# Kernel tuning notes

Hardware: AMD Instinct MI355X
Metric: run time of the kernel (lower is better)

Reference implementation:

```python
import jax, jax.numpy as jnp
import numpy as np

B, C, H, W = 2, 64, 512, 512
HEADS = 4
EPS = 1e-12  # F.normalize eps


def setup_inputs() -> dict:
    key = jax.random.key(0)
    ks = jax.random.split(key, 7)
    s = 0.02
    return {
        "x": jax.random.normal(ks[0], (B, C, H, W), jnp.float32),
        "Wq": jax.random.normal(ks[1], (C, C), jnp.float32) * s,
        "Wk": jax.random.normal(ks[2], (C, C), jnp.float32) * s,
        "Wv": jax.random.normal(ks[3], (C, C), jnp.float32) * s,
        "Wp": jax.random.normal(ks[4], (C, C), jnp.float32) * s,
        "bp": jax.random.normal(ks[5], (C,), jnp.float32) * s,
        "rescale": jnp.ones((HEADS, 1, 1), jnp.float32),
    }


def reference(x, Wq, Wk, Wv, Wp, bp, rescale):
    b, c, h, w = x.shape
    n = h * w
    d = c // HEADS
    xf = x.reshape(b, c, n)  # 1x1 conv == channel matmul on flattened spatial

    def conv1x1(Wt):
        return jnp.einsum('oc,bcn->bon', Wt, xf)

    # torch: permute->reshape(b,n,c)->split heads->transpose == reshape conv out to (b,heads,d,n)
    q = conv1x1(Wq).reshape(b, HEADS, d, n)
    k = conv1x1(Wk).reshape(b, HEADS, d, n)
    v = conv1x1(Wv).reshape(b, HEADS, d, n)

    def l2norm(t):  # F.normalize(p=2, dim=-1)
        nrm = jnp.sqrt(jnp.sum(t * t, axis=-1, keepdims=True))
        return t / jnp.maximum(nrm, EPS)

    q = l2norm(q)
    k = l2norm(k)

    attn = jnp.einsum('bhdn,bhen->bhde', k, q)  # (b, heads, d, d) tiny matrix
    attn = attn * rescale  # rescale broadcasts (heads,1,1)
    attn = jax.nn.softmax(attn, axis=-1)

    o = jnp.einsum('bhde,bhen->bhdn', attn, v).reshape(b, c, n)
    out = jnp.einsum('oc,bcn->bon', Wp, o) + bp[None, :, None] + xf  # proj + residual
    return out.reshape(b, c, h, w)
```

## Files before the change

kernel.cpp:

```cpp
#include <hip/hip_runtime.h>
#include <math.h>

#define C 64
#define NHEADS 4
#define DH 16
#define NN 262144
#define NB 2
#define PB 512
#define NT 2
#define EPS 1e-12f

typedef __attribute__((ext_vector_type(8))) short short8v;
typedef __attribute__((ext_vector_type(8))) unsigned short ushort8v;
typedef __attribute__((ext_vector_type(4))) unsigned short ushort4v;
typedef __attribute__((ext_vector_type(4))) float f32x4;

static __device__ __forceinline__ unsigned short f2bf(float f) {
  union { float f; unsigned int u; } v; v.f = f;
  unsigned int r = v.u + 0x7fffu + ((v.u >> 16) & 1u);
  return (unsigned short)(r >> 16);
}

__global__ __launch_bounds__(256, 2) void gram_kernel(const float* __restrict__ x,
                                                      float* __restrict__ Gc) {
  __shared__ unsigned short xs[C * 256];
  const int b = blockIdx.y;
  const int chunk = blockIdx.x;
  const float* xb = x + (size_t)b * C * NN;
  const int t = threadIdx.x;
  const int w = t >> 6, l = t & 63;
  const int lrow = l & 15, lhi = l >> 4;

  const int gA0 = (w >> 1) * 2, gA1 = gA0 + 1;
  const int gB0 = (w & 1) * 2,  gB1 = gB0 + 1;
  const int cA0 = gA0 * 16 + lrow, cA1 = gA1 * 16 + lrow;
  const int cB0 = gB0 * 16 + lrow, cB1 = gB1 * 16 + lrow;

  f32x4 acc0 = {0.f,0.f,0.f,0.f}, acc1 = {0.f,0.f,0.f,0.f};
  f32x4 acc2 = {0.f,0.f,0.f,0.f}, acc3 = {0.f,0.f,0.f,0.f};

  for (int tile = 0; tile < NT; ++tile) {
    const int j0 = (chunk * NT + tile) * 256;
    __syncthreads();
#pragma unroll
    for (int i = 0; i < 8; ++i) {
      const int oi = i * 256 + t;
      const int c = oi >> 5, oct = oi & 31;
      const float* src = xb + (size_t)c * NN + j0 + oct * 8;
      const float4 v0 = *reinterpret_cast<const float4*>(src);
      const float4 v1 = *reinterpret_cast<const float4*>(src + 4);
      ushort8v pk;
      pk[0] = f2bf(v0.x); pk[1] = f2bf(v0.y); pk[2] = f2bf(v0.z); pk[3] = f2bf(v0.w);
      pk[4] = f2bf(v1.x); pk[5] = f2bf(v1.y); pk[6] = f2bf(v1.z); pk[7] = f2bf(v1.w);
      *reinterpret_cast<ushort8v*>(&xs[c * 256 + ((oct ^ (c & 7)) << 3)]) = pk;
    }
    __syncthreads();
#pragma unroll
    for (int s = 0; s < 8; ++s) {
      const int o = s * 4 + lhi;
      const short8v fA0 = *reinterpret_cast<const short8v*>(&xs[cA0 * 256 + ((o ^ (cA0 & 7)) << 3)]);
      const short8v fA1 = *reinterpret_cast<const short8v*>(&xs[cA1 * 256 + ((o ^ (cA1 & 7)) << 3)]);
      const short8v fB0 = *reinterpret_cast<const short8v*>(&xs[cB0 * 256 + ((o ^ (cB0 & 7)) << 3)]);
      const short8v fB1 = *reinterpret_cast<const short8v*>(&xs[cB1 * 256 + ((o ^ (cB1 & 7)) << 3)]);
      acc0 = __builtin_amdgcn_mfma_f32_16x16x32_bf16(fA0, fB0, acc0, 0, 0, 0);
      acc1 = __builtin_amdgcn_mfma_f32_16x16x32_bf16(fA0, fB1, acc1, 0, 0, 0);
      acc2 = __builtin_amdgcn_mfma_f32_16x16x32_bf16(fA1, fB0, acc2, 0, 0, 0);
      acc3 = __builtin_amdgcn_mfma_f32_16x16x32_bf16(fA1, fB1, acc3, 0, 0, 0);
    }
  }
  float* g = Gc + ((size_t)b * PB + chunk) * 4096;
#pragma unroll
  for (int r = 0; r < 4; ++r) {
    const int row = lhi * 4 + r;
    g[(gA0 * 16 + row) * 64 + gB0 * 16 + lrow] = acc0[r];
    g[(gA0 * 16 + row) * 64 + gB1 * 16 + lrow] = acc1[r];
    g[(gA1 * 16 + row) * 64 + gB0 * 16 + lrow] = acc2[r];
    g[(gA1 * 16 + row) * 64 + gB1 * 16 + lrow] = acc3[r];
  }
}

__global__ __launch_bounds__(256) void reduce_kernel(const float* __restrict__ Gc,
                                                     float* __restrict__ G) {
  __shared__ float s[4][64];
  const int b = blockIdx.y;
  const int g = blockIdx.x;
  const int t = threadIdx.x;
  const int e = g * 64 + (t & 63);
  const int chunk = t >> 6;
  float sum = 0.f;
  for (int p = chunk; p < PB; p += 4)
    sum += Gc[((size_t)b * PB + p) * 4096 + e];
  s[chunk][t & 63] = sum;
  __syncthreads();
  if (t < 64) G[(size_t)b * 4096 + g * 64 + t] = s[0][t] + s[1][t] + s[2][t] + s[3][t];
}

__global__ __launch_bounds__(256) void attn_kernel(const float* __restrict__ G,
    const float* __restrict__ Wq, const float* __restrict__ Wk,
    const float* __restrict__ Wv, const float* __restrict__ Wp,
    const float* __restrict__ rescale, unsigned short* __restrict__ Ebf) {
  __shared__ float Gs[4096], GQt[4096], GKt[4096], T[4096];
  __shared__ float attnw[64][DH];
  __shared__ float nq[64], nk[64];
  const int b = blockIdx.x;
  const int t = threadIdx.x;

  for (int i = t; i < 4096; i += 256) Gs[i] = G[(size_t)b * 4096 + i];
  __syncthreads();
  for (int i = t; i < 4096; i += 256) {
    const int c = i >> 6, e = i & 63;
    float sq_ = 0.f, sk_ = 0.f;
    for (int c2 = 0; c2 < 64; ++c2) {
      const float g = Gs[c * 64 + c2];
      sq_ += g * Wq[e * 64 + c2];
      sk_ += g * Wk[e * 64 + c2];
    }
    GQt[c * 64 + e] = sq_;
    GKt[c * 64 + e] = sk_;
  }
  __syncthreads();
  if (t < 64) {
    float s = 0.f;
    for (int c2 = 0; c2 < 64; ++c2) s += Wq[t * 64 + c2] * GQt[c2 * 64 + t];
    nq[t] = sqrtf(fmaxf(s, 0.f));
  } else if (t < 128) {
    const int d = t - 64;
    float s = 0.f;
    for (int c2 = 0; c2 < 64; ++c2) s += Wk[d * 64 + c2] * GKt[c2 * 64 + d];
    nk[d] = sqrtf(fmaxf(s, 0.f));
  }
  __syncthreads();
  if (t < 64) {
    const int h = t >> 4;
    const float rs = rescale[h];
    const float nkd = fmaxf(nk[t], EPS);
    float logits[DH];
    float mx = -1e30f;
    for (int ee = 0; ee < DH; ++ee) {
      const int e = h * DH + ee;
      float num = 0.f;
      for (int c2 = 0; c2 < 64; ++c2) num += Wk[t * 64 + c2] * GQt[c2 * 64 + e];
      const float l = num / (nkd * fmaxf(nq[e], EPS)) * rs;
      logits[ee] = l;
      mx = fmaxf(mx, l);
    }
    float sum = 0.f;
    for (int ee = 0; ee < DH; ++ee) { const float p = expf(logits[ee] - mx); logits[ee] = p; sum += p; }
    const float inv = 1.f / sum;
    for (int ee = 0; ee < DH; ++ee) attnw[t][ee] = logits[ee] * inv;
  }
  __syncthreads();
  for (int i = t; i < 4096; i += 256) {
    const int r = i >> 6, c = i & 63;
    const int h = r >> 4;
    float s = 0.f;
    for (int e = 0; e < DH; ++e) s += attnw[r][e] * Wv[(h * DH + e) * 64 + c];
    T[i] = s;
  }
  __syncthreads();
  for (int i = t; i < 4096; i += 256) {
    const int r = i >> 6, c = i & 63;
    float s = (r == c) ? 1.f : 0.f;
    for (int m = 0; m < 64; ++m) s += Wp[r * 64 + m] * T[m * 64 + c];
    Ebf[(size_t)b * 4096 + i] = f2bf(s);
  }
}

__global__ __launch_bounds__(256, 4) void apply_kernel(const float* __restrict__ x,
    const unsigned short* __restrict__ Ebf, const float* __restrict__ bp,
    float* __restrict__ out) {
  __shared__ unsigned short xt[128 * 64];
  const int b = blockIdx.y;
  const int n0 = blockIdx.x * 128;
  const float* xb = x + (size_t)b * C * NN;
  float* ob = out + (size_t)b * C * NN;
  const int t = threadIdx.x;
  const int w = t >> 6, l = t & 63;
  const int lrow = l & 15, lhi = l >> 4;

  short8v ef[4][2];
  const unsigned short* eb = Ebf + (size_t)b * 4096;
#pragma unroll
  for (int ot = 0; ot < 4; ++ot)
#pragma unroll
    for (int ks = 0; ks < 2; ++ks)
      ef[ot][ks] = *reinterpret_cast<const short8v*>(eb + (ot * 16 + lrow) * 64 + ks * 32 + lhi * 8);

#pragma unroll
  for (int h = 0; h < 2; ++h) {
    const int n = h * 64 + l;
#pragma unroll
    for (int i = 0; i < 4; ++i) {
      const int c0 = w * 16 + i * 4;
      const float v0 = xb[(size_t)(c0 + 0) * NN + n0 + n];
      const float v1 = xb[(size_t)(c0 + 1) * NN + n0 + n];
      const float v2 = xb[(size_t)(c0 + 2) * NN + n0 + n];
      const float v3 = xb[(size_t)(c0 + 3) * NN + n0 + n];
      ushort4v pk;
      pk[0] = f2bf(v0); pk[1] = f2bf(v1); pk[2] = f2bf(v2); pk[3] = f2bf(v3);
      const int q = c0 >> 2;
      *reinterpret_cast<ushort4v*>(
          &xt[n * 64 + ((((q >> 1) ^ (n & 7)) << 3) + (q & 1) * 4)]) = pk;
    }
  }
  __syncthreads();

  f32x4 acc[4][2];
#pragma unroll
  for (int ot = 0; ot < 4; ++ot)
#pragma unroll
    for (int nn = 0; nn < 2; ++nn) acc[ot][nn] = (f32x4){0.f, 0.f, 0.f, 0.f};

  const int nbase = w * 32;
#pragma unroll
  for (int nn = 0; nn < 2; ++nn) {
    const int n = nbase + nn * 16 + lrow;
#pragma unroll
    for (int ks = 0; ks < 2; ++ks) {
      const int s = ks * 4 + lhi;
      const short8v xf = *reinterpret_cast<const short8v*>(&xt[n * 64 + ((s ^ (n & 7)) << 3)]);
#pragma unroll
      for (int ot = 0; ot < 4; ++ot)
        acc[ot][nn] = __builtin_amdgcn_mfma_f32_16x16x32_bf16(ef[ot][ks], xf, acc[ot][nn], 0, 0, 0);
    }
  }

#pragma unroll
  for (int ot = 0; ot < 4; ++ot) {
#pragma unroll
    for (int r = 0; r < 4; ++r) {
      const int o = ot * 16 + lhi * 4 + r;
      const float bias = bp[o];
#pragma unroll
      for (int nn = 0; nn < 2; ++nn) {
        const int n = nbase + nn * 16 + lrow;
        ob[(size_t)o * NN + n0 + n] = acc[ot][nn][r] + bias;
      }
    }
  }
}

extern "C" void kernel_launch(void* const* d_in, const int* in_sizes, int n_in,
                              void* d_out, int out_size, void* d_ws, size_t ws_size,
                              hipStream_t stream) {
  const float* x       = (const float*)d_in[0];
  const float* Wq      = (const float*)d_in[1];
  const float* Wk      = (const float*)d_in[2];
  const float* Wv      = (const float*)d_in[3];
  const float* Wp      = (const float*)d_in[4];
  const float* bp      = (const float*)d_in[5];
  const float* rescale = (const float*)d_in[6];
  float* out = (float*)d_out;

  float* Gc = out;
  float* G  = (float*)d_ws;
  unsigned short* Ebf = (unsigned short*)(G + (size_t)NB * 4096);

  gram_kernel<<<dim3(PB, NB), dim3(256), 0, stream>>>(x, Gc);
  reduce_kernel<<<dim3(64, NB), dim3(256), 0, stream>>>(Gc, G);
  attn_kernel<<<dim3(NB), dim3(256), 0, stream>>>(G, Wq, Wk, Wv, Wp, rescale, Ebf);
  apply_kernel<<<dim3(2048, NB), dim3(256), 0, stream>>>(x, Ebf, bp, out);
}
```

Baseline: 155.7 us.

## Rewrite apply kernel as persistent per-wave streaming without LDS staging

Replaces the LDS-staged apply kernel with a grid-stride persistent kernel in which each wave handles 32-pixel chunks. Inputs are loaded straight into MFMA operand registers, and the operand order is swapped so that the accumulator layout allows float4 vectorized output stores. This removes the shared-memory transpose and the block barrier, and cuts the grid to 384x2 blocks. In exchange, the per-lane global loads are 4-byte strided across channels, each covering only 16 contiguous pixels, which may hurt coalescing. Occupancy is lower because the launch bound drops from 4 to 3 blocks.

```diff
diff --git a/kernel.cpp b/kernel.cpp
--- a/kernel.cpp
+++ b/kernel.cpp
@@ -12,7 +12,6 @@
 
 typedef __attribute__((ext_vector_type(8))) short short8v;
 typedef __attribute__((ext_vector_type(8))) unsigned short ushort8v;
-typedef __attribute__((ext_vector_type(4))) unsigned short ushort4v;
 typedef __attribute__((ext_vector_type(4))) float f32x4;
 
 static __device__ __forceinline__ unsigned short f2bf(float f) {
@@ -166,12 +165,10 @@
   }
 }
 
-__global__ __launch_bounds__(256, 4) void apply_kernel(const float* __restrict__ x,
+__global__ __launch_bounds__(256, 3) void apply_stream(const float* __restrict__ x,
     const unsigned short* __restrict__ Ebf, const float* __restrict__ bp,
     float* __restrict__ out) {
-  __shared__ unsigned short xt[128 * 64];
   const int b = blockIdx.y;
-  const int n0 = blockIdx.x * 128;
   const float* xb = x + (size_t)b * C * NN;
   float* ob = out + (size_t)b * C * NN;
   const int t = threadIdx.x;
@@ -186,55 +183,51 @@
     for (int ks = 0; ks < 2; ++ks)
       ef[ot][ks] = *reinterpret_cast<const short8v*>(eb + (ot * 16 + lrow) * 64 + ks * 32 + lhi * 8);
 
-#pragma unroll
-  for (int h = 0; h < 2; ++h) {
-    const int n = h * 64 + l;
-#pragma unroll
-    for (int i = 0; i < 4; ++i) {
-      const int c0 = w * 16 + i * 4;
-      const float v0 = xb[(size_t)(c0 + 0) * NN + n0 + n];
-      const float v1 = xb[(size_t)(c0 + 1) * NN + n0 + n];
-      const float v2 = xb[(size_t)(c0 + 2) * NN + n0 + n];
-      const float v3 = xb[(size_t)(c0 + 3) * NN + n0 + n];
-      ushort4v pk;
-      pk[0] = f2bf(v0); pk[1] = f2bf(v1); pk[2] = f2bf(v2); pk[3] = f2bf(v3);
-      const int q = c0 >> 2;
-      *reinterpret_cast<ushort4v*>(
-          &xt[n * 64 + ((((q >> 1) ^ (n & 7)) << 3) + (q & 1) * 4)]) = pk;
-    }
-  }
-  __syncthreads();
-
-  f32x4 acc[4][2];
-#pragma unroll
-  for (int ot = 0; ot < 4; ++ot)
-#pragma unroll
-    for (int nn = 0; nn < 2; ++nn) acc[ot][nn] = (f32x4){0.f, 0.f, 0.f, 0.f};
-
-  const int nbase = w * 32;
-#pragma unroll
-  for (int nn = 0; nn < 2; ++nn) {
-    const int n = nbase + nn * 16 + lrow;
-#pragma unroll
-    for (int ks = 0; ks < 2; ++ks) {
-      const int s = ks * 4 + lhi;
-      const short8v xf = *reinterpret_cast<const short8v*>(&xt[n * 64 + ((s ^ (n & 7)) << 3)]);
-#pragma unroll
-      for (int ot = 0; ot < 4; ++ot)
-        acc[ot][nn] = __builtin_amdgcn_mfma_f32_16x16x32_bf16(ef[ot][ks], xf, acc[ot][nn], 0, 0, 0);
-    }
-  }
-
-#pragma unroll
-  for (int ot = 0; ot < 4; ++ot) {
-#pragma unroll
-    for (int r = 0; r < 4; ++r) {
-      const int o = ot * 16 + lhi * 4 + r;
-      const float bias = bp[o];
+  float bias[4];
+#pragma unroll
+  for (int ot = 0; ot < 4; ++ot) bias[ot] = bp[ot * 16 + lrow];
+
+  const int gw = blockIdx.x * 4 + w;
+  const int NW = gridDim.x * 4;
+
+  for (int ch = gw; ch < NN / 32; ch += NW) {
+    const int n0 = ch * 32;
+    short8v xf[2][2];
+#pragma unroll
+    for (int nn = 0; nn < 2; ++nn) {
+      const int n = n0 + nn * 16 + lrow;
+#pragma unroll
+      for (int ks = 0; ks < 2; ++ks) {
+        const float* src = xb + (size_t)(ks * 32 + lhi * 8) * NN + n;
+        ushort8v pk;
+#pragma unroll
+        for (int j = 0; j < 8; ++j) pk[j] = f2bf(src[(size_t)j * NN]);
+        xf[nn][ks] = *reinterpret_cast<short8v*>(&pk);
+      }
+    }
+    f32x4 acc[4][2];
+#pragma unroll
+    for (int ot = 0; ot < 4; ++ot)
+#pragma unroll
+      for (int nn = 0; nn < 2; ++nn) acc[ot][nn] = (f32x4){0.f, 0.f, 0.f, 0.f};
+#pragma unroll
+    for (int nn = 0; nn < 2; ++nn)
+#pragma unroll
+      for (int ks = 0; ks < 2; ++ks)
+#pragma unroll
+        for (int ot = 0; ot < 4; ++ot)
+          acc[ot][nn] = __builtin_amdgcn_mfma_f32_16x16x32_bf16(xf[nn][ks], ef[ot][ks], acc[ot][nn], 0, 0, 0);
+#pragma unroll
+    for (int ot = 0; ot < 4; ++ot) {
+      const int o = ot * 16 + lrow;
 #pragma unroll
       for (int nn = 0; nn < 2; ++nn) {
-        const int n = nbase + nn * 16 + lrow;
-        ob[(size_t)o * NN + n0 + n] = acc[ot][nn][r] + bias;
+        float4 o4;
+        o4.x = acc[ot][nn][0] + bias[ot];
+        o4.y = acc[ot][nn][1] + bias[ot];
+        o4.z = acc[ot][nn][2] + bias[ot];
+        o4.w = acc[ot][nn][3] + bias[ot];
+        *reinterpret_cast<float4*>(&ob[(size_t)o * NN + n0 + nn * 16 + lhi * 4]) = o4;
       }
     }
   }
@@ -259,5 +252,5 @@
   gram_kernel<<<dim3(PB, NB), dim3(256), 0, stream>>>(x, Gc);
   reduce_kernel<<<dim3(64, NB), dim3(256), 0, stream>>>(Gc, G);
   attn_kernel<<<dim3(NB), dim3(256), 0, stream>>>(G, Wq, Wk, Wv, Wp, rescale, Ebf);
-  apply_kernel<<<dim3(2048, NB), dim3(256), 0, stream>>>(x, Ebf, bp, out);
-}
+  apply_stream<<<dim3(384, NB), dim3(256), 0, stream>>>(x, Ebf, bp, out);
+}
```

After: 157.8 us. No clear change (+1.3%).
